# Performance work log

Hardware: AMD Instinct MI355X
Metric: run time of the kernel (lower is better)

Reference implementation:

```python
import jax, jax.numpy as jnp
import numpy as np

B, H0, W0, C, NH, WS, SHIFT = 32, 48, 48, 384, 12, 12, 6
N = WS * WS
TAB = 2 * WS - 1  # 23


def _window_partition(x, ws):
    b, h, w, c = x.shape
    x = x.reshape(b, h // ws, ws, w // ws, ws, c)
    return x.transpose(0, 1, 3, 2, 4, 5).reshape(-1, ws, ws, c)


def _window_reverse(win, ws, h, w):
    b = win.shape[0] // (h * w // ws // ws)
    x = win.reshape(b, h // ws, w // ws, ws, ws, -1)
    return x.transpose(0, 1, 3, 2, 4, 5).reshape(b, h, w, -1)


def _ln(y, g, b):
    m = y.mean(-1, keepdims=True)
    v = y.var(-1, keepdims=True)
    return (y - m) * jax.lax.rsqrt(v + 1e-5) * g + b


def setup_inputs() -> dict:
    key = jax.random.key(0)
    ks = jax.random.split(key, 12)
    s = 0.02
    # relative coords table, normalized to [-1, 1]
    rng = np.arange(-(WS - 1), WS, dtype=np.float32) / (WS - 1)
    table = np.stack(np.meshgrid(rng, rng, indexing='ij'), axis=-1)[None]  # (1,23,23,2)
    # relative position index
    ch, cw = np.meshgrid(np.arange(WS), np.arange(WS), indexing='ij')
    coords = np.stack([ch, cw]).reshape(2, -1)
    rel = coords[:, :, None] - coords[:, None, :] + (WS - 1)
    rpi = (rel[0] * TAB + rel[1]).astype(np.int32)  # (N,N)
    # shifted-window attention mask
    img = np.zeros((1, H0, W0, 1), dtype=np.float32)
    cnt = 0
    sl = (slice(0, -WS), slice(-WS, -SHIFT), slice(-SHIFT, None))
    for hs in sl:
        for ws_ in sl:
            img[:, hs, ws_, :] = cnt
            cnt += 1
    mw = img.reshape(1, H0 // WS, WS, W0 // WS, WS, 1).transpose(0, 1, 3, 2, 4, 5).reshape(-1, N)
    diff = mw[:, None, :] - mw[:, :, None]
    attn_mask = np.where(diff != 0, -100.0, 0.0).astype(np.float32)  # (nW,N,N)
    Ch = C * 4
    return {
        'x': jax.random.normal(ks[0], (B, H0 * W0, C), jnp.float32),
        'relative_coords_table': jnp.asarray(table),
        'relative_position_index': jnp.asarray(rpi),
        'attn_mask': jnp.asarray(attn_mask),
        'qkv_w': jax.random.normal(ks[1], (C, 3 * C), jnp.float32) * s,
        'q_bias': jnp.zeros((C,), jnp.float32),
        'v_bias': jnp.zeros((C,), jnp.float32),
        'logit_scale': jnp.log(10.0 * jnp.ones((NH, 1, 1), jnp.float32)),
        'cpb_w1': jax.random.normal(ks[2], (2, 512), jnp.float32) * s,
        'cpb_b1': jnp.zeros((512,), jnp.float32),
        'cpb_w2': jax.random.normal(ks[3], (512, NH), jnp.float32) * s,
        'proj_w': jax.random.normal(ks[4], (C, C), jnp.float32) * s,
        'proj_b': jnp.zeros((C,), jnp.float32),
        'norm1_g': jnp.ones((C,), jnp.float32),
        'norm1_b': jnp.zeros((C,), jnp.float32),
        'norm2_g': jnp.ones((C,), jnp.float32),
        'norm2_b': jnp.zeros((C,), jnp.float32),
        'fc1_w': jax.random.normal(ks[5], (C, Ch), jnp.float32) * s,
        'fc1_b': jnp.zeros((Ch,), jnp.float32),
        'fc2_w': jax.random.normal(ks[6], (Ch, C), jnp.float32) * s,
        'fc2_b': jnp.zeros((C,), jnp.float32),
        'H': H0,
        'W': W0,
    }


def reference(x, relative_coords_table, relative_position_index, attn_mask,
              qkv_w, q_bias, v_bias, logit_scale, cpb_w1, cpb_b1, cpb_w2,
              proj_w, proj_b, norm1_g, norm1_b, norm2_g, norm2_b,
              fc1_w, fc1_b, fc2_w, fc2_b, H, W):
    b, L, c = x.shape
    hd = c // NH
    shortcut = x
    x4 = x.reshape(b, H, W, c)
    shifted = jnp.roll(x4, (-SHIFT, -SHIFT), axis=(1, 2))
    xw = _window_partition(shifted, WS).reshape(-1, N, c)  # (B_, N, C)
    qkv_bias = jnp.concatenate([q_bias, jnp.zeros_like(q_bias), v_bias])
    qkv = xw @ qkv_w + qkv_bias
    qkv = qkv.reshape(-1, N, 3, NH, hd).transpose(2, 0, 3, 1, 4)  # (3,B_,h,N,d)
    q, k, v = qkv[0], qkv[1], qkv[2]
    qn = q / jnp.maximum(jnp.linalg.norm(q, axis=-1, keepdims=True), 1e-12)
    kn = k / jnp.maximum(jnp.linalg.norm(k, axis=-1, keepdims=True), 1e-12)
    attn = jnp.einsum('bhnd,bhmd->bhnm', qn, kn)
    scale = jnp.exp(jnp.minimum(logit_scale, jnp.log(100.0)))  # clamp max=log(1/0.01)
    attn = attn * scale
    tab = jax.nn.relu(relative_coords_table @ cpb_w1 + cpb_b1) @ cpb_w2  # (1,23,23,h)
    tab = tab.reshape(-1, NH)
    bias = tab[relative_position_index.reshape(-1)].reshape(N, N, NH).transpose(2, 0, 1)
    bias = 16.0 * jax.nn.sigmoid(bias)
    attn = attn + bias[None]
    nW = attn_mask.shape[0]
    attn = attn.reshape(b, nW, NH, N, N) + attn_mask[None, :, None]
    attn = jax.nn.softmax(attn.reshape(-1, NH, N, N), axis=-1)
    out = jnp.einsum('bhnm,bhmd->bhnd', attn, v).transpose(0, 2, 1, 3).reshape(-1, N, c)
    out = out @ proj_w + proj_b
    out = _window_reverse(out.reshape(-1, WS, WS, c), WS, H, W)
    x4 = jnp.roll(out, (SHIFT, SHIFT), axis=(1, 2)).reshape(b, H * W, c)
    x = shortcut + _ln(x4, norm1_g, norm1_b)
    h = jax.nn.gelu(x @ fc1_w + fc1_b, approximate=False) @ fc2_w + fc2_b
    x = x + _ln(h, norm2_g, norm2_b)
    return x
```

## Files before the change

kernel.cpp:

```cpp
#include <hip/hip_runtime.h>


typedef unsigned int uint32;
typedef unsigned short u16;
typedef __attribute__((ext_vector_type(4))) float f32x4;
typedef __attribute__((ext_vector_type(8))) __bf16 bf16x8;

#define LOG2E 1.4426950408889634f

static __device__ __forceinline__ u16 f2bf(float f) {
    union { __bf16 b; u16 u; } v; v.b = (__bf16)f; return v.u;
}
static __device__ __forceinline__ uint32 pack2(float a, float b) {
    union { __bf16 h[2]; uint32 u; } v;
    v.h[0] = (__bf16)a; v.h[1] = (__bf16)b; return v.u;
}
static __device__ __forceinline__ float blo(uint32 u){ union{uint32 u;float f;}v; v.u=u<<16; return v.f; }
static __device__ __forceinline__ float bhi(uint32 u){ union{uint32 u;float f;}v; v.u=u&0xffff0000u; return v.f; }

typedef __attribute__((address_space(1))) const void gas_void;
typedef __attribute__((address_space(3))) void las_void;
static __device__ __forceinline__ void glds16(const void* g, void* l) {
    __builtin_amdgcn_global_load_lds((gas_void*)g, (las_void*)l, 16, 0, 0);
}

#define SWZ(c, row) ((c) ^ ((((row) >> 1) & 3) << 3))

#define VMCNT(N) asm volatile("s_waitcnt vmcnt(" #N ")" ::: "memory")
#define BARM() do { asm volatile("" ::: "memory"); __builtin_amdgcn_s_barrier(); asm volatile("" ::: "memory"); } while (0)

static __device__ __forceinline__ float fast_gelu(float x) {
    float x2 = x * x;
    float w = x * fmaf(0.10294842f, x2, 2.30226005f);
    float e = exp2f(w);
    float r = __builtin_amdgcn_rcpf(e + 1.0f);
    return fmaf(-x, r, x);
}


__global__ void wt_convert(const float* __restrict__ W, u16* __restrict__ WT, int K, int N) {
    long idx = (long)blockIdx.x * 256 + threadIdx.x;
    long tot = (long)K * N;
    if (idx >= tot) return;
    int n = (int)(idx / K), k = (int)(idx - (long)n * K);
    WT[(long)n * K + SWZ(k, n)] = f2bf(W[(long)k * N + n]);
}

__global__ void build_qkv_bias(const float* __restrict__ qb, const float* __restrict__ vb,
                               float* __restrict__ outb) {
    int c = blockIdx.x * 256 + threadIdx.x;
    if (c >= 1152) return;
    outb[c] = (c < 384) ? qb[c] : ((c < 768) ? 0.f : vb[c - 768]);
}

__global__ void cpb_tab(const float* __restrict__ table, const float* __restrict__ w1,
                        const float* __restrict__ b1, const float* __restrict__ w2,
                        float* __restrict__ tab) {
    __shared__ float hid[512];
    int e = blockIdx.x;
    float tx = table[e * 2 + 0], ty = table[e * 2 + 1];
    for (int u = threadIdx.x; u < 512; u += 256)
        hid[u] = fmaxf(tx * w1[u] + ty * w1[512 + u] + b1[u], 0.f);
    __syncthreads();
    if (threadIdx.x < 12) {
        float s = 0.f;
        for (int u = 0; u < 512; ++u) s += hid[u] * w2[u * 12 + threadIdx.x];
        tab[e * 12 + threadIdx.x] = s;
    }
}

__global__ void build_bm(const float* __restrict__ tab, const int* __restrict__ rpi,
                         const float* __restrict__ mask, float* __restrict__ bm) {
    int idx = blockIdx.x * 256 + threadIdx.x;
    if (idx >= 12 * 16 * 20736) return;
    int h = idx / 331776, rem = idx - h * 331776;
    int wim = rem / 20736, ij = rem - wim * 20736;
    float t = tab[rpi[ij] * 12 + h];
    float bias = 16.f / (1.f + __expf(-t));
    bm[idx] = (bias + mask[wim * 20736 + ij]) * LOG2E;
}

__global__ void gather_xbf(const float* __restrict__ x, u16* __restrict__ xw) {
    int idx = blockIdx.x * 256 + threadIdx.x;
    if (idx >= 73728 * 48) return;
    int row = idx / 48, c = (idx - row * 48) * 8;
    int win = row / 144, n = row - win * 144;
    int b = win >> 4, wi = win & 15;
    int r = n / 12, cc = n - r * 12;
    int sh = ((wi >> 2) * 12 + r + 6) % 48;
    int sw = ((wi & 3) * 12 + cc + 6) % 48;
    long src = ((long)(b * 2304 + sh * 48 + sw)) * 384 + c;
    float4 f0 = *(const float4*)(x + src);
    float4 f1 = *(const float4*)(x + src + 4);
    uint4 o;
    o.x = pack2(f0.x, f0.y); o.y = pack2(f0.z, f0.w);
    o.z = pack2(f1.x, f1.y); o.w = pack2(f1.z, f1.w);
    *(uint4*)(xw + (long)row * 384 + SWZ(c, row)) = o;
}


enum { EPI_PLAIN = 1, EPI_GELU = 2 };

template<int EPI, bool OSWZ, int NK>
__global__ __launch_bounds__(256, 2) void gemm_k(
    const u16* __restrict__ Ag, const u16* __restrict__ Bg,
    const float* __restrict__ bias, u16* __restrict__ outp,
    int N, int ntn)
{
    constexpr int K = NK * 32;
    extern __shared__ u16 lds[];
    u16* As = lds;
    u16* Bs = lds + 24576;

    const int tid = threadIdx.x, lane = tid & 63, wid = tid >> 6;
    const int qq = gridDim.x >> 3;
    const int wg = (blockIdx.x & 7) * qq + (blockIdx.x >> 3);
    const int mIdx = wg / ntn, nIdx = wg - mIdx * ntn;
    const int m0 = mIdx << 8, n0 = nIdx << 7;

    const int wrow = wid << 6;
    const int fr = lane & 15, gsel = lane >> 4;

    const int srow = (wid << 4) + (lane >> 2);
    const int scol = (lane & 3) << 3;
    const u16* aP[4];
    const u16* bP[2];
#pragma unroll
    for (int q = 0; q < 4; ++q) aP[q] = Ag + (long)(m0 + (q << 6) + srow) * K + scol;
#pragma unroll
    for (int q = 0; q < 2; ++q) bP[q] = Bg + (long)(n0 + (q << 6) + srow) * K + scol;

    auto stage = [&](int buf, int kt) {
#pragma unroll
        for (int q = 0; q < 4; ++q)
            glds16(aP[q] + (kt << 5), &As[buf * 8192 + ((q << 6) + (wid << 4)) * 32]);
#pragma unroll
        for (int q = 0; q < 2; ++q)
            glds16(bP[q] + (kt << 5), &Bs[buf * 4096 + ((q << 6) + (wid << 4)) * 32]);
    };

    int arow[4], acol[4], brow[8], bcol[8];
#pragma unroll
    for (int i = 0; i < 4; ++i) {
        arow[i] = wrow + i * 16 + fr;
        acol[i] = (gsel ^ ((arow[i] >> 1) & 3)) << 3;
    }
#pragma unroll
    for (int j = 0; j < 8; ++j) {
        brow[j] = j * 16 + fr;
        bcol[j] = (gsel ^ ((brow[j] >> 1) & 3)) << 3;
    }

    f32x4 acc[4][8];
    const f32x4 zero4 = {0.f, 0.f, 0.f, 0.f};
#pragma unroll
    for (int i = 0; i < 4; ++i)
#pragma unroll
        for (int j = 0; j < 8; ++j) acc[i][j] = zero4;

    auto compute = [&](int buf) {
        const u16* pa = As + buf * 8192;
        const u16* pb = Bs + buf * 4096;
        bf16x8 af[4], bg[8];
#pragma unroll
        for (int i = 0; i < 4; ++i) af[i] = *(const bf16x8*)&pa[arow[i] * 32 + acol[i]];
#pragma unroll
        for (int j = 0; j < 8; ++j) bg[j] = *(const bf16x8*)&pb[brow[j] * 32 + bcol[j]];
#pragma unroll
        for (int i = 0; i < 4; ++i)
#pragma unroll
            for (int j = 0; j < 8; ++j)
                acc[i][j] = __builtin_amdgcn_mfma_f32_16x16x32_bf16(af[i], bg[j], acc[i][j], 0, 0, 0);
    };

    stage(0, 0);
    stage(1, 1);
#define GITER(KT, BC, BN_) \
    VMCNT(6); BARM(); stage(BN_, (KT) + 2); compute(BC);
    for (int g = 0; g < (NK - 1) / 3; ++g) {
        const int kb = g * 3;
        GITER(kb + 0, 0, 2);
        GITER(kb + 1, 1, 0);
        GITER(kb + 2, 2, 1);
    }
#undef GITER
    VMCNT(6); BARM(); stage(2, NK - 1); compute(0);
    VMCNT(6); BARM(); compute(1);
    VMCNT(0); BARM(); compute(2);

    const int rbase = gsel << 2;
    float bv[8];
#pragma unroll
    for (int j = 0; j < 8; ++j) bv[j] = bias[n0 + j * 16 + fr];
#pragma unroll
    for (int i = 0; i < 4; ++i) {
#pragma unroll
        for (int r = 0; r < 4; ++r) {
            const int gm = m0 + wrow + i * 16 + rbase + r;
            u16* orow = outp + (long)gm * N;
            const int sx = OSWZ ? (((gm >> 1) & 3) << 3) : 0;
#pragma unroll
            for (int j = 0; j < 8; ++j) {
                const int gn = n0 + j * 16 + fr;
                float v = acc[i][j][r] + bv[j];
                if constexpr (EPI == EPI_GELU) v = fast_gelu(v);
                orow[gn ^ sx] = f2bf(v);
            }
        }
    }
}


__global__ __launch_bounds__(192) void attn_k(
    const u16* __restrict__ qkv,
    const float* __restrict__ bm,
    const float* __restrict__ lsc,
    u16* __restrict__ attn_o)
{
    __shared__ __align__(16) u16 KL[144][40];
    __shared__ __align__(16) u16 VT[32][168];
    __shared__ __align__(16) u16 PL[3][16][168];
    const int blk = blockIdx.x;
    const int win = blk / 12, head = blk - win * 12;
    const int tid = threadIdx.x, lane = tid & 63, wid = tid >> 6;
    const u16* Qp = qkv + (long)win * 144 * 1152 + head * 32;
    const u16* Kp = Qp + 384;
    const u16* Vp = Qp + 768;
    const float scale = __expf(fminf(lsc[head], 4.6051701859880914f)) * LOG2E;
    const float* bmp = bm + ((long)head * 16 + (win & 15)) * 20736;

    if (tid < 144) {
        const uint4* s = (const uint4*)(Kp + (long)tid * 1152);
        uint4 uu[4] = { s[0], s[1], s[2], s[3] };
        float f[32];
#pragma unroll
        for (int q = 0; q < 4; ++q) {
            f[q*8+0]=blo(uu[q].x); f[q*8+1]=bhi(uu[q].x);
            f[q*8+2]=blo(uu[q].y); f[q*8+3]=bhi(uu[q].y);
            f[q*8+4]=blo(uu[q].z); f[q*8+5]=bhi(uu[q].z);
            f[q*8+6]=blo(uu[q].w); f[q*8+7]=bhi(uu[q].w);
        }
        float ss = 0.f;
#pragma unroll
        for (int i = 0; i < 32; ++i) ss += f[i] * f[i];
        float inv = 1.f / fmaxf(sqrtf(ss), 1e-12f);
        uint32 pk[16];
#pragma unroll
        for (int i = 0; i < 16; ++i) pk[i] = pack2(f[2*i] * inv, f[2*i+1] * inv);
        uint4* d = (uint4*)&KL[tid][0];
        d[0] = make_uint4(pk[0], pk[1], pk[2], pk[3]);
        d[1] = make_uint4(pk[4], pk[5], pk[6], pk[7]);
        d[2] = make_uint4(pk[8], pk[9], pk[10], pk[11]);
        d[3] = make_uint4(pk[12], pk[13], pk[14], pk[15]);
        const uint4* sv = (const uint4*)(Vp + (long)tid * 1152);
        uint4 vv[4] = { sv[0], sv[1], sv[2], sv[3] };
        u16 vs[32];
#pragma unroll
        for (int q = 0; q < 4; ++q) {
            vs[q*8+0] = (u16)(vv[q].x & 0xffffu); vs[q*8+1] = (u16)(vv[q].x >> 16);
            vs[q*8+2] = (u16)(vv[q].y & 0xffffu); vs[q*8+3] = (u16)(vv[q].y >> 16);
            vs[q*8+4] = (u16)(vv[q].z & 0xffffu); vs[q*8+5] = (u16)(vv[q].z >> 16);
            vs[q*8+6] = (u16)(vv[q].w & 0xffffu); vs[q*8+7] = (u16)(vv[q].w >> 16);
        }
#pragma unroll
        for (int d2 = 0; d2 < 32; ++d2) VT[d2][tid] = vs[d2];
    }
    for (int idx = tid; idx < 512; idx += 192) VT[idx >> 4][144 + (idx & 15)] = 0;
    __syncthreads();

    const int fr = lane & 15, fk = (lane >> 4) << 3, rb = (lane >> 4) << 2;
    const f32x4 zero4 = {0.f, 0.f, 0.f, 0.f};

    for (int s = wid; s < 9; s += 3) {
        const uint4 qu = *(const uint4*)(Qp + (long)(s * 16 + fr) * 1152 + fk);
        float qf[8];
        qf[0]=blo(qu.x); qf[1]=bhi(qu.x); qf[2]=blo(qu.y); qf[3]=bhi(qu.y);
        qf[4]=blo(qu.z); qf[5]=bhi(qu.z); qf[6]=blo(qu.w); qf[7]=bhi(qu.w);
        float ss = 0.f;
#pragma unroll
        for (int i = 0; i < 8; ++i) ss += qf[i] * qf[i];
        ss += __shfl_xor(ss, 16);
        ss += __shfl_xor(ss, 32);
        float qinv = scale / fmaxf(sqrtf(ss), 1e-12f);
        union { uint32 u[4]; bf16x8 v; } cv;
#pragma unroll
        for (int i = 0; i < 4; ++i) cv.u[i] = pack2(qf[2*i] * qinv, qf[2*i+1] * qinv);
        bf16x8 aq = cv.v;

        f32x4 sacc[9];
#pragma unroll
        for (int jt = 0; jt < 9; ++jt) sacc[jt] = zero4;
#pragma unroll
        for (int jt = 0; jt < 9; ++jt) {
            bf16x8 bk = *(const bf16x8*)&KL[jt * 16 + fr][fk];
            sacc[jt] = __builtin_amdgcn_mfma_f32_16x16x32_bf16(aq, bk, sacc[jt], 0, 0, 0);
        }
        float mx[4] = {-1e30f, -1e30f, -1e30f, -1e30f};
#pragma unroll
        for (int jt = 0; jt < 9; ++jt) {
            int gj = jt * 16 + fr;
#pragma unroll
            for (int r = 0; r < 4; ++r) {
                int gi = s * 16 + rb + r;
                float v = sacc[jt][r] + bmp[gi * 144 + gj];
                sacc[jt][r] = v;
                mx[r] = fmaxf(mx[r], v);
            }
        }
#pragma unroll
        for (int r = 0; r < 4; ++r) {
#pragma unroll
            for (int o = 1; o < 16; o <<= 1) mx[r] = fmaxf(mx[r], __shfl_xor(mx[r], o));
        }
        float sm[4] = {0.f, 0.f, 0.f, 0.f};
#pragma unroll
        for (int jt = 0; jt < 9; ++jt)
#pragma unroll
            for (int r = 0; r < 4; ++r) {
                float e = exp2f(sacc[jt][r] - mx[r]);
                sacc[jt][r] = e;
                sm[r] += e;
            }
#pragma unroll
        for (int r = 0; r < 4; ++r) {
#pragma unroll
            for (int o = 1; o < 16; o <<= 1) sm[r] += __shfl_xor(sm[r], o);
            sm[r] = 1.f / sm[r];
        }
#pragma unroll
        for (int jt = 0; jt < 9; ++jt)
#pragma unroll
            for (int r = 0; r < 4; ++r)
                PL[wid][rb + r][jt * 16 + fr] = f2bf(sacc[jt][r]);
#pragma unroll
        for (int r = 0; r < 4; ++r) PL[wid][rb + r][144 + fr] = 0;

        f32x4 oa0 = zero4, oa1 = zero4;
#pragma unroll
        for (int kt = 0; kt < 5; ++kt) {
            bf16x8 ap  = *(const bf16x8*)&PL[wid][fr][kt * 32 + fk];
            bf16x8 bv0 = *(const bf16x8*)&VT[fr][kt * 32 + fk];
            bf16x8 bv1 = *(const bf16x8*)&VT[16 + fr][kt * 32 + fk];
            oa0 = __builtin_amdgcn_mfma_f32_16x16x32_bf16(ap, bv0, oa0, 0, 0, 0);
            oa1 = __builtin_amdgcn_mfma_f32_16x16x32_bf16(ap, bv1, oa1, 0, 0, 0);
        }
#pragma unroll
        for (int r = 0; r < 4; ++r) {
            long row = (long)win * 144 + s * 16 + rb + r;
            int c0 = head * 32 + fr, c1 = head * 32 + 16 + fr;
            attn_o[row * 384 + SWZ(c0, row)] = f2bf(oa0[r] * sm[r]);
            attn_o[row * 384 + SWZ(c1, row)] = f2bf(oa1[r] * sm[r]);
        }
    }
}


__global__ __launch_bounds__(256) void ln1_k(
    const u16* __restrict__ pin, const float* __restrict__ x,
    const float* __restrict__ g, const float* __restrict__ bb,
    u16* __restrict__ y1b)
{
    const int token = blockIdx.x * 4 + (threadIdx.x >> 6);
    const int lane = threadIdx.x & 63;
    int b = token / 2304, hw = token - b * 2304;
    int h = hw / 48, w = hw - h * 48;
    int sh = h + 42; if (sh >= 48) sh -= 48;
    int sw = w + 42; if (sw >= 48) sw -= 48;
    int wh = sh / 12, r = sh - wh * 12;
    int ww = sw / 12, cc = sw - ww * 12;
    long srow = (long)(b * 16 + wh * 4 + ww) * 144 + r * 12 + cc;
    const u16* src = pin + srow * 384;
    const int c0 = lane * 4, c1 = 256 + lane * 2;
    uint2 p0 = *(const uint2*)(src + c0);
    uint32 p1 = *(const uint32*)(src + c1);
    float v[6] = { blo(p0.x), bhi(p0.x), blo(p0.y), bhi(p0.y), blo(p1), bhi(p1) };
    float s1 = 0.f, s2 = 0.f;
#pragma unroll
    for (int i = 0; i < 6; ++i) { s1 += v[i]; s2 += v[i] * v[i]; }
#pragma unroll
    for (int o = 1; o < 64; o <<= 1) { s1 += __shfl_xor(s1, o); s2 += __shfl_xor(s2, o); }
    float mean = s1 * (1.f / 384.f);
    float var = s2 * (1.f / 384.f) - mean * mean;
    float rs = rsqrtf(var + 1e-5f);
    const float* xx = x + (long)token * 384;
    float4 r0 = *(const float4*)(xx + c0);
    float2 r1 = *(const float2*)(xx + c1);
    float4 g0 = *(const float4*)(g + c0);
    float2 g1 = *(const float2*)(g + c1);
    float4 b0 = *(const float4*)(bb + c0);
    float2 b1 = *(const float2*)(bb + c1);
    float o0 = r0.x + (v[0] - mean) * rs * g0.x + b0.x;
    float o1 = r0.y + (v[1] - mean) * rs * g0.y + b0.y;
    float o2 = r0.z + (v[2] - mean) * rs * g0.z + b0.z;
    float o3 = r0.w + (v[3] - mean) * rs * g0.w + b0.w;
    float o4 = r1.x + (v[4] - mean) * rs * g1.x + b1.x;
    float o5 = r1.y + (v[5] - mean) * rs * g1.y + b1.y;
    u16* oo = y1b + (long)token * 384;
    const int sx = ((token >> 1) & 3) << 3;
    uint2 w0; w0.x = pack2(o0, o1); w0.y = pack2(o2, o3);
    *(uint2*)(oo + (c0 ^ sx)) = w0;
    *(uint32*)(oo + (c1 ^ sx)) = pack2(o4, o5);
}

__global__ __launch_bounds__(256) void ln2_k(
    const u16* __restrict__ t2, const u16* __restrict__ y1b,
    const float* __restrict__ g, const float* __restrict__ bb,
    float* __restrict__ outp)
{
    const int token = blockIdx.x * 4 + (threadIdx.x >> 6);
    const int lane = threadIdx.x & 63;
    const int c0 = lane * 4, c1 = 256 + lane * 2;
    const u16* src = t2 + (long)token * 384;
    uint2 p0 = *(const uint2*)(src + c0);
    uint32 p1 = *(const uint32*)(src + c1);
    float v[6] = { blo(p0.x), bhi(p0.x), blo(p0.y), bhi(p0.y), blo(p1), bhi(p1) };
    float s1 = 0.f, s2 = 0.f;
#pragma unroll
    for (int i = 0; i < 6; ++i) { s1 += v[i]; s2 += v[i] * v[i]; }
#pragma unroll
    for (int o = 1; o < 64; o <<= 1) { s1 += __shfl_xor(s1, o); s2 += __shfl_xor(s2, o); }
    float mean = s1 * (1.f / 384.f);
    float var = s2 * (1.f / 384.f) - mean * mean;
    float rs = rsqrtf(var + 1e-5f);
    const u16* rr = y1b + (long)token * 384;
    const int sx = ((token >> 1) & 3) << 3;
    uint2 q0 = *(const uint2*)(rr + (c0 ^ sx));
    uint32 q1 = *(const uint32*)(rr + (c1 ^ sx));
    float4 g0 = *(const float4*)(g + c0);
    float2 g1 = *(const float2*)(g + c1);
    float4 b0 = *(const float4*)(bb + c0);
    float2 b1 = *(const float2*)(bb + c1);
    float* oo = outp + (long)token * 384;
    float4 w0;
    w0.x = blo(q0.x) + (v[0] - mean) * rs * g0.x + b0.x;
    w0.y = bhi(q0.x) + (v[1] - mean) * rs * g0.y + b0.y;
    w0.z = blo(q0.y) + (v[2] - mean) * rs * g0.z + b0.z;
    w0.w = bhi(q0.y) + (v[3] - mean) * rs * g0.w + b0.w;
    float2 w1;
    w1.x = blo(q1) + (v[4] - mean) * rs * g1.x + b1.x;
    w1.y = bhi(q1) + (v[5] - mean) * rs * g1.y + b1.y;
    *(float4*)(oo + c0) = w0;
    *(float2*)(oo + c1) = w1;
}


extern "C" void kernel_launch(void* const* d_in, const int* in_sizes, int n_in,
                              void* d_out, int out_size, void* d_ws, size_t ws_size,
                              hipStream_t stream) {
    (void)in_sizes; (void)n_in; (void)out_size; (void)ws_size;
    const float* x      = (const float*)d_in[0];
    const float* table  = (const float*)d_in[1];
    const int*   rpi    = (const int*)d_in[2];
    const float* mask   = (const float*)d_in[3];
    const float* qkv_w  = (const float*)d_in[4];
    const float* q_bias = (const float*)d_in[5];
    const float* v_bias = (const float*)d_in[6];
    const float* lsc    = (const float*)d_in[7];
    const float* cpb_w1 = (const float*)d_in[8];
    const float* cpb_b1 = (const float*)d_in[9];
    const float* cpb_w2 = (const float*)d_in[10];
    const float* proj_w = (const float*)d_in[11];
    const float* proj_b = (const float*)d_in[12];
    const float* n1g    = (const float*)d_in[13];
    const float* n1b    = (const float*)d_in[14];
    const float* n2g    = (const float*)d_in[15];
    const float* n2b    = (const float*)d_in[16];
    const float* fc1_w  = (const float*)d_in[17];
    const float* fc1_b  = (const float*)d_in[18];
    const float* fc2_w  = (const float*)d_in[19];
    const float* fc2_b  = (const float*)d_in[20];
    float* outp = (float*)d_out;

    char* ws = (char*)d_ws;
    const size_t offA    = 0;
    const size_t offB    = 226492416;
    const size_t offC    = offB + 56623104;
    const size_t offBM   = offC + 56623104;
    const size_t offTab  = offBM + 15925248;
    const size_t offQW   = offTab + 25600;
    const size_t offPW   = offQW + 884736;
    const size_t offF1   = offPW + 294912;
    const size_t offF2   = offF1 + 1179648;
    const size_t offQB   = offF2 + 1179648;

    u16*   qkvb    = (u16*)(ws + offA);
    u16*   proj_o  = (u16*)(ws + offA);
    u16*   hbuf    = (u16*)(ws + offA);
    u16*   attn_o  = (u16*)(ws + offB);
    u16*   t2      = (u16*)(ws + offB);
    u16*   xw      = (u16*)(ws + offC);
    u16*   y1b     = (u16*)(ws + offC);
    float* bm      = (float*)(ws + offBM);
    float* tab     = (float*)(ws + offTab);
    u16*   qkv_wT  = (u16*)(ws + offQW);
    u16*   proj_wT = (u16*)(ws + offPW);
    u16*   fc1_wT  = (u16*)(ws + offF1);
    u16*   fc2_wT  = (u16*)(ws + offF2);
    float* qkvbias = (float*)(ws + offQB);

    hipFuncSetAttribute((const void*)&gemm_k<EPI_PLAIN, false, 12>,
                        hipFuncAttributeMaxDynamicSharedMemorySize, 73728);
    hipFuncSetAttribute((const void*)&gemm_k<EPI_GELU, true, 12>,
                        hipFuncAttributeMaxDynamicSharedMemorySize, 73728);
    hipFuncSetAttribute((const void*)&gemm_k<EPI_PLAIN, false, 48>,
                        hipFuncAttributeMaxDynamicSharedMemorySize, 73728);

    wt_convert<<<(384 * 1152 + 255) / 256, 256, 0, stream>>>(qkv_w, qkv_wT, 384, 1152);
    wt_convert<<<(384 * 384 + 255) / 256, 256, 0, stream>>>(proj_w, proj_wT, 384, 384);
    wt_convert<<<(384 * 1536 + 255) / 256, 256, 0, stream>>>(fc1_w, fc1_wT, 384, 1536);
    wt_convert<<<(1536 * 384 + 255) / 256, 256, 0, stream>>>(fc2_w, fc2_wT, 1536, 384);
    build_qkv_bias<<<5, 256, 0, stream>>>(q_bias, v_bias, qkvbias);
    cpb_tab<<<529, 256, 0, stream>>>(table, cpb_w1, cpb_b1, cpb_w2, tab);
    build_bm<<<(12 * 16 * 20736 + 255) / 256, 256, 0, stream>>>(tab, rpi, mask, bm);
    gather_xbf<<<(73728 * 48 + 255) / 256, 256, 0, stream>>>(x, xw);

    gemm_k<EPI_PLAIN, false, 12><<<288 * 9, 256, 73728, stream>>>(xw, qkv_wT, qkvbias, qkvb, 1152, 9);

    attn_k<<<6144, 192, 0, stream>>>(qkvb, bm, lsc, attn_o);

    gemm_k<EPI_PLAIN, false, 12><<<288 * 3, 256, 73728, stream>>>(attn_o, proj_wT, proj_b, proj_o, 384, 3);

    ln1_k<<<18432, 256, 0, stream>>>(proj_o, x, n1g, n1b, y1b);

    gemm_k<EPI_GELU, true, 12><<<288 * 12, 256, 73728, stream>>>(y1b, fc1_wT, fc1_b, hbuf, 1536, 12);

    gemm_k<EPI_PLAIN, false, 48><<<288 * 3, 256, 73728, stream>>>(hbuf, fc2_wT, fc2_b, t2, 384, 3);

    ln2_k<<<18432, 256, 0, stream>>>(t2, y1b, n2g, n2b, outp);
}
```

Baseline: 702.6 us.

## Switch GEMM to double-buffered static LDS pipeline with full vmcnt waits

The GEMM kernel's triple-buffered dynamic-LDS pipeline (two stages in flight, vmcnt(6) waits) becomes a double-buffered loop on static shared arrays that waits for all outstanding loads each k-step. This cuts LDS per block from 72KB to 48KB and simplifies the loop, which could allow more resident blocks per CU. In exchange, prefetch depth drops to one stage, so global-load latency is hidden less well, and register limits from launch_bounds(256,2) may keep occupancy unchanged anyway.

```diff
diff --git a/kernel.cpp b/kernel.cpp
--- a/kernel.cpp
+++ b/kernel.cpp
@@ -108,9 +108,8 @@
     int N, int ntn)
 {
     constexpr int K = NK * 32;
-    extern __shared__ u16 lds[];
-    u16* As = lds;
-    u16* Bs = lds + 24576;
+    __shared__ __align__(16) u16 As[2][8192];
+    __shared__ __align__(16) u16 Bs[2][4096];
 
     const int tid = threadIdx.x, lane = tid & 63, wid = tid >> 6;
     const int qq = gridDim.x >> 3;
@@ -133,10 +132,10 @@
     auto stage = [&](int buf, int kt) {
 #pragma unroll
         for (int q = 0; q < 4; ++q)
-            glds16(aP[q] + (kt << 5), &As[buf * 8192 + ((q << 6) + (wid << 4)) * 32]);
+            glds16(aP[q] + (kt << 5), &As[buf][((q << 6) + (wid << 4)) * 32]);
 #pragma unroll
         for (int q = 0; q < 2; ++q)
-            glds16(bP[q] + (kt << 5), &Bs[buf * 4096 + ((q << 6) + (wid << 4)) * 32]);
+            glds16(bP[q] + (kt << 5), &Bs[buf][((q << 6) + (wid << 4)) * 32]);
     };
 
     int arow[4], acol[4], brow[8], bcol[8];
@@ -159,8 +158,8 @@
         for (int j = 0; j < 8; ++j) acc[i][j] = zero4;
 
     auto compute = [&](int buf) {
-        const u16* pa = As + buf * 8192;
-        const u16* pb = Bs + buf * 4096;
+        const u16* pa = &As[buf][0];
+        const u16* pb = &Bs[buf][0];
         bf16x8 af[4], bg[8];
 #pragma unroll
         for (int i = 0; i < 4; ++i) af[i] = *(const bf16x8*)&pa[arow[i] * 32 + acol[i]];
@@ -174,19 +173,12 @@
     };
 
     stage(0, 0);
-    stage(1, 1);
-#define GITER(KT, BC, BN_) \
-    VMCNT(6); BARM(); stage(BN_, (KT) + 2); compute(BC);
-    for (int g = 0; g < (NK - 1) / 3; ++g) {
-        const int kb = g * 3;
-        GITER(kb + 0, 0, 2);
-        GITER(kb + 1, 1, 0);
-        GITER(kb + 2, 2, 1);
-    }
-#undef GITER
-    VMCNT(6); BARM(); stage(2, NK - 1); compute(0);
-    VMCNT(6); BARM(); compute(1);
-    VMCNT(0); BARM(); compute(2);
+#pragma unroll
+    for (int t = 0; t < NK; ++t) {
+        VMCNT(0); BARM();
+        if (t + 1 < NK) stage((t + 1) & 1, t + 1);
+        compute(t & 1);
+    }
 
     const int rbase = gsel << 2;
     float bv[8];
@@ -498,13 +490,6 @@
     u16*   fc2_wT  = (u16*)(ws + offF2);
     float* qkvbias = (float*)(ws + offQB);
 
-    hipFuncSetAttribute((const void*)&gemm_k<EPI_PLAIN, false, 12>,
-                        hipFuncAttributeMaxDynamicSharedMemorySize, 73728);
-    hipFuncSetAttribute((const void*)&gemm_k<EPI_GELU, true, 12>,
-                        hipFuncAttributeMaxDynamicSharedMemorySize, 73728);
-    hipFuncSetAttribute((const void*)&gemm_k<EPI_PLAIN, false, 48>,
-                        hipFuncAttributeMaxDynamicSharedMemorySize, 73728);
-
     wt_convert<<<(384 * 1152 + 255) / 256, 256, 0, stream>>>(qkv_w, qkv_wT, 384, 1152);
     wt_convert<<<(384 * 384 + 255) / 256, 256, 0, stream>>>(proj_w, proj_wT, 384, 384);
     wt_convert<<<(384 * 1536 + 255) / 256, 256, 0, stream>>>(fc1_w, fc1_wT, 384, 1536);
@@ -514,17 +499,17 @@
     build_bm<<<(12 * 16 * 20736 + 255) / 256, 256, 0, stream>>>(tab, rpi, mask, bm);
     gather_xbf<<<(73728 * 48 + 255) / 256, 256, 0, stream>>>(x, xw);
 
-    gemm_k<EPI_PLAIN, false, 12><<<288 * 9, 256, 73728, stream>>>(xw, qkv_wT, qkvbias, qkvb, 1152, 9);
+    gemm_k<EPI_PLAIN, false, 12><<<288 * 9, 256, 0, stream>>>(xw, qkv_wT, qkvbias, qkvb, 1152, 9);
 
     attn_k<<<6144, 192, 0, stream>>>(qkvb, bm, lsc, attn_o);
 
-    gemm_k<EPI_PLAIN, false, 12><<<288 * 3, 256, 73728, stream>>>(attn_o, proj_wT, proj_b, proj_o, 384, 3);
+    gemm_k<EPI_PLAIN, false, 12><<<288 * 3, 256, 0, stream>>>(attn_o, proj_wT, proj_b, proj_o, 384, 3);
 
     ln1_k<<<18432, 256, 0, stream>>>(proj_o, x, n1g, n1b, y1b);
 
-    gemm_k<EPI_GELU, true, 12><<<288 * 12, 256, 73728, stream>>>(y1b, fc1_wT, fc1_b, hbuf, 1536, 12);
-
-    gemm_k<EPI_PLAIN, false, 48><<<288 * 3, 256, 73728, stream>>>(hbuf, fc2_wT, fc2_b, t2, 384, 3);
+    gemm_k<EPI_GELU, true, 12><<<288 * 12, 256, 0, stream>>>(y1b, fc1_wT, fc1_b, hbuf, 1536, 12);
+
+    gemm_k<EPI_PLAIN, false, 48><<<288 * 3, 256, 0, stream>>>(hbuf, fc2_wT, fc2_b, t2, 384, 3);
 
     ln2_k<<<18432, 256, 0, stream>>>(t2, y1b, n2g, n2b, outp);
 }
```

Result: no change. 710.5 us (+1.1%).

## Transpose attention score layout and add MFMA priority hints

Applied to the files above, without the earlier changes.

The attention kernel now computes S^T by swapping the MFMA operands, so each lane owns one query row. That reduces the softmax max/sum reductions to two cross-lane shuffles instead of four per-row butterfly reductions. The bias/mask table is stored transposed so the per-lane loads match the new layout, and P is written to LDS in the matching orientation. The PV and output paths are adjusted to match. s_setprio hints are also wrapped around the MFMA blocks in both the GEMM and attention kernels to favour matrix issue.

```diff
diff --git a/kernel.cpp b/kernel.cpp
--- a/kernel.cpp
+++ b/kernel.cpp
@@ -70,14 +70,16 @@
 }
 
 __global__ void build_bm(const float* __restrict__ tab, const int* __restrict__ rpi,
-                         const float* __restrict__ mask, float* __restrict__ bm) {
+                         const float* __restrict__ mask, float* __restrict__ bmT) {
     int idx = blockIdx.x * 256 + threadIdx.x;
     if (idx >= 12 * 16 * 20736) return;
     int h = idx / 331776, rem = idx - h * 331776;
-    int wim = rem / 20736, ij = rem - wim * 20736;
+    int wim = rem / 20736, ji = rem - wim * 20736;
+    int j = ji / 144, i = ji - j * 144;
+    int ij = i * 144 + j;
     float t = tab[rpi[ij] * 12 + h];
     float bias = 16.f / (1.f + __expf(-t));
-    bm[idx] = (bias + mask[wim * 20736 + ij]) * LOG2E;
+    bmT[idx] = (bias + mask[wim * 20736 + ij]) * LOG2E;
 }
 
 __global__ void gather_xbf(const float* __restrict__ x, u16* __restrict__ xw) {
@@ -166,11 +168,13 @@
         for (int i = 0; i < 4; ++i) af[i] = *(const bf16x8*)&pa[arow[i] * 32 + acol[i]];
 #pragma unroll
         for (int j = 0; j < 8; ++j) bg[j] = *(const bf16x8*)&pb[brow[j] * 32 + bcol[j]];
+        __builtin_amdgcn_s_setprio(1);
 #pragma unroll
         for (int i = 0; i < 4; ++i)
 #pragma unroll
             for (int j = 0; j < 8; ++j)
                 acc[i][j] = __builtin_amdgcn_mfma_f32_16x16x32_bf16(af[i], bg[j], acc[i][j], 0, 0, 0);
+        __builtin_amdgcn_s_setprio(0);
     };
 
     stage(0, 0);
@@ -213,7 +217,7 @@
 
 __global__ __launch_bounds__(192) void attn_k(
     const u16* __restrict__ qkv,
-    const float* __restrict__ bm,
+    const float* __restrict__ bmT,
     const float* __restrict__ lsc,
     u16* __restrict__ attn_o)
 {
@@ -227,7 +231,7 @@
     const u16* Kp = Qp + 384;
     const u16* Vp = Qp + 768;
     const float scale = __expf(fminf(lsc[head], 4.6051701859880914f)) * LOG2E;
-    const float* bmp = bm + ((long)head * 16 + (win & 15)) * 20736;
+    const float* bmp = bmT + ((long)head * 16 + (win & 15)) * 20736;
 
     if (tid < 144) {
         const uint4* s = (const uint4*)(Kp + (long)tid * 1152);
@@ -272,7 +276,8 @@
     const f32x4 zero4 = {0.f, 0.f, 0.f, 0.f};
 
     for (int s = wid; s < 9; s += 3) {
-        const uint4 qu = *(const uint4*)(Qp + (long)(s * 16 + fr) * 1152 + fk);
+        const int s16 = s * 16;
+        const uint4 qu = *(const uint4*)(Qp + (long)(s16 + fr) * 1152 + fk);
         float qf[8];
         qf[0]=blo(qu.x); qf[1]=bhi(qu.x); qf[2]=blo(qu.y); qf[3]=bhi(qu.y);
         qf[4]=blo(qu.z); qf[5]=bhi(qu.z); qf[6]=blo(qu.w); qf[7]=bhi(qu.w);
@@ -290,66 +295,66 @@
         f32x4 sacc[9];
 #pragma unroll
         for (int jt = 0; jt < 9; ++jt) sacc[jt] = zero4;
+        __builtin_amdgcn_s_setprio(1);
 #pragma unroll
         for (int jt = 0; jt < 9; ++jt) {
             bf16x8 bk = *(const bf16x8*)&KL[jt * 16 + fr][fk];
-            sacc[jt] = __builtin_amdgcn_mfma_f32_16x16x32_bf16(aq, bk, sacc[jt], 0, 0, 0);
-        }
-        float mx[4] = {-1e30f, -1e30f, -1e30f, -1e30f};
+            sacc[jt] = __builtin_amdgcn_mfma_f32_16x16x32_bf16(bk, aq, sacc[jt], 0, 0, 0);
+        }
+        __builtin_amdgcn_s_setprio(0);
+
+        float mx = -1e30f;
 #pragma unroll
         for (int jt = 0; jt < 9; ++jt) {
-            int gj = jt * 16 + fr;
 #pragma unroll
             for (int r = 0; r < 4; ++r) {
-                int gi = s * 16 + rb + r;
-                float v = sacc[jt][r] + bmp[gi * 144 + gj];
+                float v = sacc[jt][r] + bmp[(jt * 16 + rb + r) * 144 + s16 + fr];
                 sacc[jt][r] = v;
-                mx[r] = fmaxf(mx[r], v);
+                mx = fmaxf(mx, v);
             }
         }
+        mx = fmaxf(mx, __shfl_xor(mx, 16));
+        mx = fmaxf(mx, __shfl_xor(mx, 32));
+        float sm = 0.f;
+#pragma unroll
+        for (int jt = 0; jt < 9; ++jt)
+#pragma unroll
+            for (int r = 0; r < 4; ++r) {
+                float e = exp2f(sacc[jt][r] - mx);
+                sacc[jt][r] = e;
+                sm += e;
+            }
+        sm += __shfl_xor(sm, 16);
+        sm += __shfl_xor(sm, 32);
+        sm = 1.f / sm;
+
+#pragma unroll
+        for (int jt = 0; jt < 9; ++jt)
+#pragma unroll
+            for (int r = 0; r < 4; ++r)
+                PL[wid][fr][jt * 16 + rb + r] = f2bf(sacc[jt][r]);
+#pragma unroll
+        for (int r = 0; r < 4; ++r) PL[wid][fr][144 + rb + r] = 0;
+
+        f32x4 oa0 = zero4, oa1 = zero4;
+        __builtin_amdgcn_s_setprio(1);
+#pragma unroll
+        for (int kt = 0; kt < 5; ++kt) {
+            bf16x8 bp  = *(const bf16x8*)&PL[wid][fr][kt * 32 + fk];
+            bf16x8 av0 = *(const bf16x8*)&VT[fr][kt * 32 + fk];
+            bf16x8 av1 = *(const bf16x8*)&VT[16 + fr][kt * 32 + fk];
+            oa0 = __builtin_amdgcn_mfma_f32_16x16x32_bf16(av0, bp, oa0, 0, 0, 0);
+            oa1 = __builtin_amdgcn_mfma_f32_16x16x32_bf16(av1, bp, oa1, 0, 0, 0);
+        }
+        __builtin_amdgcn_s_setprio(0);
+
+        const long row = (long)win * 144 + s16 + fr;
+        u16* orow = attn_o + row * 384;
 #pragma unroll
         for (int r = 0; r < 4; ++r) {
-#pragma unroll
-            for (int o = 1; o < 16; o <<= 1) mx[r] = fmaxf(mx[r], __shfl_xor(mx[r], o));
-        }
-        float sm[4] = {0.f, 0.f, 0.f, 0.f};
-#pragma unroll
-        for (int jt = 0; jt < 9; ++jt)
-#pragma unroll
-            for (int r = 0; r < 4; ++r) {
-                float e = exp2f(sacc[jt][r] - mx[r]);
-                sacc[jt][r] = e;
-                sm[r] += e;
-            }
-#pragma unroll
-        for (int r = 0; r < 4; ++r) {
-#pragma unroll
-            for (int o = 1; o < 16; o <<= 1) sm[r] += __shfl_xor(sm[r], o);
-            sm[r] = 1.f / sm[r];
-        }
-#pragma unroll
-        for (int jt = 0; jt < 9; ++jt)
-#pragma unroll
-            for (int r = 0; r < 4; ++r)
-                PL[wid][rb + r][jt * 16 + fr] = f2bf(sacc[jt][r]);
-#pragma unroll
-        for (int r = 0; r < 4; ++r) PL[wid][rb + r][144 + fr] = 0;
-
-        f32x4 oa0 = zero4, oa1 = zero4;
-#pragma unroll
-        for (int kt = 0; kt < 5; ++kt) {
-            bf16x8 ap  = *(const bf16x8*)&PL[wid][fr][kt * 32 + fk];
-            bf16x8 bv0 = *(const bf16x8*)&VT[fr][kt * 32 + fk];
-            bf16x8 bv1 = *(const bf16x8*)&VT[16 + fr][kt * 32 + fk];
-            oa0 = __builtin_amdgcn_mfma_f32_16x16x32_bf16(ap, bv0, oa0, 0, 0, 0);
-            oa1 = __builtin_amdgcn_mfma_f32_16x16x32_bf16(ap, bv1, oa1, 0, 0, 0);
-        }
-#pragma unroll
-        for (int r = 0; r < 4; ++r) {
-            long row = (long)win * 144 + s * 16 + rb + r;
-            int c0 = head * 32 + fr, c1 = head * 32 + 16 + fr;
-            attn_o[row * 384 + SWZ(c0, row)] = f2bf(oa0[r] * sm[r]);
-            attn_o[row * 384 + SWZ(c1, row)] = f2bf(oa1[r] * sm[r]);
+            int c0 = head * 32 + rb + r, c1 = c0 + 16;
+            orow[SWZ(c0, row)] = f2bf(oa0[r] * sm);
+            orow[SWZ(c1, row)] = f2bf(oa1[r] * sm);
         }
     }
 }
@@ -490,7 +495,7 @@
     u16*   t2      = (u16*)(ws + offB);
     u16*   xw      = (u16*)(ws + offC);
     u16*   y1b     = (u16*)(ws + offC);
-    float* bm      = (float*)(ws + offBM);
+    float* bmT     = (float*)(ws + offBM);
     float* tab     = (float*)(ws + offTab);
     u16*   qkv_wT  = (u16*)(ws + offQW);
     u16*   proj_wT = (u16*)(ws + offPW);
@@ -511,12 +516,12 @@
     wt_convert<<<(1536 * 384 + 255) / 256, 256, 0, stream>>>(fc2_w, fc2_wT, 1536, 384);
     build_qkv_bias<<<5, 256, 0, stream>>>(q_bias, v_bias, qkvbias);
     cpb_tab<<<529, 256, 0, stream>>>(table, cpb_w1, cpb_b1, cpb_w2, tab);
-    build_bm<<<(12 * 16 * 20736 + 255) / 256, 256, 0, stream>>>(tab, rpi, mask, bm);
+    build_bm<<<(12 * 16 * 20736 + 255) / 256, 256, 0, stream>>>(tab, rpi, mask, bmT);
     gather_xbf<<<(73728 * 48 + 255) / 256, 256, 0, stream>>>(x, xw);
 
     gemm_k<EPI_PLAIN, false, 12><<<288 * 9, 256, 73728, stream>>>(xw, qkv_wT, qkvbias, qkvb, 1152, 9);
 
-    attn_k<<<6144, 192, 0, stream>>>(qkvb, bm, lsc, attn_o);
+    attn_k<<<6144, 192, 0, stream>>>(qkvb, bmT, lsc, attn_o);
 
     gemm_k<EPI_PLAIN, false, 12><<<288 * 3, 256, 73728, stream>>>(attn_o, proj_wT, proj_b, proj_o, 384, 3);
 
```

Measured after the change: 726.5 us. 1.03x slower.
